# Kernel optimization log

Measured on AMD Instinct MI355X. Metric: run time of the kernel, lower is better.

## Reference

```python
import jax, jax.numpy as jnp
import numpy as np

D = 300      # embedding / model dim
H = 150      # LSTM hidden per direction (dim // 2)
V = 21257    # vocab size
B, S = 1024, 256


def _lstm_run(x, lengths, Wih, Whh, b):
    """Unidirectional masked LSTM. x: [B,S,Din]; outputs [B,S,H].
    State frozen and output zeroed at t >= lengths (packed-sequence semantics)."""
    Bb, Ss, _ = x.shape
    h0 = jnp.zeros((Bb, H), x.dtype)
    c0 = jnp.zeros((Bb, H), x.dtype)

    def step(carry, inp):
        h, c = carry
        xt, t = inp
        g = xt @ Wih.T + h @ Whh.T + b          # [B, 4H]
        i, f, gg, o = jnp.split(g, 4, axis=-1)   # torch gate order i,f,g,o
        i = jax.nn.sigmoid(i); f = jax.nn.sigmoid(f)
        gg = jnp.tanh(gg); o = jax.nn.sigmoid(o)
        c_new = f * c + i * gg
        h_new = o * jnp.tanh(c_new)
        valid = (t < lengths)[:, None]
        h2 = jnp.where(valid, h_new, h)
        c2 = jnp.where(valid, c_new, c)
        return (h2, c2), jnp.where(valid, h_new, jnp.zeros_like(h_new))

    _, ys = jax.lax.scan(step, (h0, c0), (jnp.swapaxes(x, 0, 1), jnp.arange(Ss)))
    return jnp.swapaxes(ys, 0, 1)


def _reverse_valid(x, lengths):
    """Reverse the valid prefix of each sequence; self-inverse on valid region."""
    Ss = x.shape[1]
    t = jnp.arange(Ss)[None, :]
    L = lengths[:, None]
    idx = jnp.where(t < L, L - 1 - t, t)
    return jnp.take_along_axis(x, idx[:, :, None], axis=1)


def _bilstm(x, lengths, pf, pb):
    hf = _lstm_run(x, lengths, *pf)
    hb = _reverse_valid(_lstm_run(_reverse_valid(x, lengths), lengths, *pb), lengths)
    return jnp.concatenate([hf, hb], axis=-1)  # [B,S,2H]


def setup_inputs() -> dict:
    key = jax.random.key(0)
    ks = jax.random.split(key, 20)
    x = jax.random.randint(ks[0], (B, S), 0, V)
    lengths = jax.random.randint(ks[1], (B,), 1, S + 1)
    mask = (jnp.arange(S)[None, :] < lengths[:, None]).astype(jnp.int64)

    def p(k, shape):
        return jax.random.normal(k, shape, dtype=jnp.float32) * 0.05

    emb = p(ks[2], (V, D))
    inp = {"x": x, "mask": mask, "emb": emb}
    # layer 0: input D; layer 1: input 2H (=D)
    names = [("l0f", D), ("l0b", D), ("l1f", 2 * H), ("l1b", 2 * H)]
    ki = 3
    for nm, din in names:
        inp[f"Wih_{nm}"] = p(ks[ki], (4 * H, din)); ki += 1
        inp[f"Whh_{nm}"] = p(ks[ki], (4 * H, H)); ki += 1
        inp[f"b_{nm}"] = p(ks[ki], (4 * H,)); ki += 1
    inp["W1"] = p(ks[15], (D, D)); inp["b1"] = p(ks[16], (D,))
    inp["W2"] = p(ks[17], (D, D)); inp["b2"] = p(ks[18], (D,))
    return inp


def reference(x, mask, emb,
              Wih_l0f, Whh_l0f, b_l0f, Wih_l0b, Whh_l0b, b_l0b,
              Wih_l1f, Whh_l1f, b_l1f, Wih_l1b, Whh_l1b, b_l1b,
              W1, b1, W2, b2):
    lengths = jnp.sum(mask != 0, axis=1)
    emb_z = emb.at[0].set(0.0)                 # padding_idx=0
    xe = emb_z[x]                              # [B,S,D]
    h1 = _bilstm(xe, lengths, (Wih_l0f, Whh_l0f, b_l0f), (Wih_l0b, Whh_l0b, b_l0b))
    h2 = _bilstm(h1, lengths, (Wih_l1f, Whh_l1f, b_l1f), (Wih_l1b, Whh_l1b, b_l1b))
    # gather output at last valid timestep (fwd last step || bwd first step)
    last = jnp.take_along_axis(h2, (lengths - 1)[:, None, None], axis=1)[:, 0, :]  # [B,300]
    # dropout is identity in eval mode
    out = jnp.tanh(last @ W1.T + b1)
    out = out @ W2.T + b2
    return out
```

## Files before the change

### kernel.cpp

```cpp
#include <hip/hip_runtime.h>

typedef unsigned short u16;
typedef __bf16 bf16x8 __attribute__((ext_vector_type(8)));
typedef float f32x4 __attribute__((ext_vector_type(4)));
typedef float f4 __attribute__((ext_vector_type(4)));
typedef unsigned short u16x8 __attribute__((ext_vector_type(8)));
typedef unsigned short u16x4 __attribute__((ext_vector_type(4)));

#define BB 1024
#define SS 256
#define DD 300
#define HH 150
#define GG 600
#define VV 21257
#define VPAD 21376
#define KSTR 320
#define GSTR 600
#define WK 160

static __device__ __forceinline__ float bf2f(u16 u){
  unsigned v = ((unsigned)u) << 16;
  return __builtin_bit_cast(float, v);
}
static __device__ __forceinline__ u16 f2bf(float f){
  unsigned u = __builtin_bit_cast(unsigned, f);
  u = u + 0x7FFFu + ((u >> 16) & 1u);
  return (u16)(u >> 16);
}
static __device__ __forceinline__ float fsig(float x){
  return __builtin_amdgcn_rcpf(1.0f + __expf(-x));
}
static __device__ __forceinline__ float ftanh_(float x){
  return 2.0f * __builtin_amdgcn_rcpf(1.0f + __expf(-2.0f*x)) - 1.0f;
}

__global__ void k_len(const int* __restrict__ mask, int* __restrict__ len){
  __shared__ int red[256];
  int b = blockIdx.x, t = threadIdx.x;
  red[t] = (mask[b*SS + t] != 0) ? 1 : 0;
  __syncthreads();
  for (int o = 128; o > 0; o >>= 1){
    if (t < o) red[t] += red[t+o];
    __syncthreads();
  }
  if (t == 0) len[b] = red[0];
}

__global__ void k_sort(const int* __restrict__ len, int* __restrict__ perm){
  __shared__ int L[1024];
  int b = threadIdx.x;
  int l = len[b];
  L[b] = l;
  __syncthreads();
  int r = 0;
  for (int j = 0; j < 1024; ++j){
    int lj = L[j];
    r += (lj < l) || (lj == l && j < b);
  }
  perm[r] = b;
}

struct PrepW {
  const float* src[8];
  u16* dst[8];
  int R[8], C[8], DR[8], DC[8];
};
__global__ void k_prepw(PrepW p){
  int z = blockIdx.y;
  int n = p.DR[z]*p.DC[z];
  for (int i = blockIdx.x*256 + threadIdx.x; i < n; i += 800*256){
    int r = i / p.DC[z], c = i - r*p.DC[z];
    float v = (r < p.R[z] && c < p.C[z]) ? p.src[z][r*p.C[z] + c] : 0.f;
    p.dst[z][i] = f2bf(v);
  }
}
struct PrepB { const float* src[4]; float* dst[4]; };
__global__ void k_prepb(PrepB p){
  int z = blockIdx.y;
  int i = blockIdx.x*256 + threadIdx.x;
  if (i < 640) p.dst[z][i] = (i < GG) ? p.src[z][i] : 0.f;
}

__global__ void k_prepemb(const float* __restrict__ emb, u16* __restrict__ dst){
  long i = (long)blockIdx.x*256 + threadIdx.x;
  if (i >= (long)VPAD*KSTR) return;
  int r = (int)(i / KSTR), c = (int)(i - (long)r*KSTR);
  float v = (r >= 1 && r < VV && c < DD) ? emb[(size_t)r*DD + c] : 0.f;
  dst[i] = f2bf(v);
}

__launch_bounds__(512, 2)
__global__ void k_gemm(const u16* __restrict__ A,
                       const u16* __restrict__ Wf, const u16* __restrict__ Wb,
                       const float* __restrict__ bsf, const float* __restrict__ bsb,
                       u16* __restrict__ of, u16* __restrict__ ob)
{
  const u16* W = blockIdx.z ? Wb : Wf;
  const float* bias = blockIdx.z ? bsb : bsf;
  u16* outp = blockIdx.z ? ob : of;

  __shared__ u16 Al[128*40];
  __shared__ u16 Bl[320*40];

  int tid = threadIdx.x;
  int l = tid & 63, w = tid >> 6;
  int lo = l & 15, hi = l >> 4;
  int wm = w >> 2, wn = w & 3;
  int m0 = blockIdx.x * 128;
  int n0 = blockIdx.y * 320;

  int ar = tid >> 2, ac = (tid & 3) * 8;
  const u16* Arow = A + (size_t)(m0 + ar)*KSTR + ac;
  bool bvld[3]; int brr[3], bcc[3];
  const u16* Brow[3];
  #pragma unroll
  for (int i = 0; i < 3; ++i){
    int ch = tid + i*512;
    bvld[i] = (ch < 1280);
    int r2 = bvld[i] ? (ch >> 2) : 0;
    brr[i] = r2; bcc[i] = (ch & 3) * 8;
    Brow[i] = W + (size_t)(n0 + r2)*KSTR + bcc[i];
  }

  u16x8 ra = *(const u16x8*)Arow;
  u16x8 rbv[3];
  #pragma unroll
  for (int i = 0; i < 3; ++i) if (bvld[i]) rbv[i] = *(const u16x8*)Brow[i];

  f32x4 zero = {0.f, 0.f, 0.f, 0.f};
  f32x4 acc[4][5];
  #pragma unroll
  for (int a = 0; a < 4; ++a)
    #pragma unroll
    for (int b = 0; b < 5; ++b) acc[a][b] = zero;

  for (int kk = 0; kk < 10; ++kk){
    __syncthreads();
    *(u16x8*)&Al[ar*40 + ac] = ra;
    #pragma unroll
    for (int i = 0; i < 3; ++i)
      if (bvld[i]) *(u16x8*)&Bl[brr[i]*40 + bcc[i]] = rbv[i];
    __syncthreads();
    if (kk < 9){
      int k1 = (kk+1)*32;
      ra = *(const u16x8*)(Arow + k1);
      #pragma unroll
      for (int i = 0; i < 3; ++i)
        if (bvld[i]) rbv[i] = *(const u16x8*)(Brow[i] + k1);
    }
    u16x8 av[4], bv[5];
    #pragma unroll
    for (int mt = 0; mt < 4; ++mt)
      av[mt] = *(const u16x8*)&Al[(wm*64 + mt*16 + lo)*40 + hi*8];
    #pragma unroll
    for (int nt = 0; nt < 5; ++nt)
      bv[nt] = *(const u16x8*)&Bl[(wn*80 + nt*16 + lo)*40 + hi*8];
    #pragma unroll
    for (int mt = 0; mt < 4; ++mt)
      #pragma unroll
      for (int nt = 0; nt < 5; ++nt)
        acc[mt][nt] = __builtin_amdgcn_mfma_f32_16x16x32_bf16(
            __builtin_bit_cast(bf16x8, av[mt]),
            __builtin_bit_cast(bf16x8, bv[nt]),
            acc[mt][nt], 0, 0, 0);
  }

  #pragma unroll
  for (int mt = 0; mt < 4; ++mt){
    #pragma unroll
    for (int nt = 0; nt < 5; ++nt){
      int col = n0 + wn*80 + nt*16 + lo;
      if (col < GG){
        float bsv = bias[col];
        int g = (col >= 450) ? 3 : (col >= 300) ? 2 : (col >= 150) ? 1 : 0;
        int cofs = (col - g*150)*4 + g;
        #pragma unroll
        for (int r = 0; r < 4; ++r){
          int row = m0 + wm*64 + mt*16 + hi*4 + r;
          outp[(size_t)row*GSTR + cofs] = f2bf(acc[mt][nt][r] + bsv);
        }
      }
    }
  }
}

#define PREF(GB, TT)                                                            \
  {                                                                             \
    _Pragma("unroll")                                                           \
    for (int r = 0; r < 4; ++r){                                                \
      int Li = Lr[r];                                                           \
      int tt = ((TT) < Li) ? (TT) : (Li-1);                                     \
      int s_ = dir ? (Li-1-tt) : tt;                                            \
      int tok = (int)tks[(hi*4+r)*256 + s_];                                    \
      int rowi = isL1 ? (rowb[r] + s_) : tok;                                   \
      GB[r] = *(const u16x4*)(xg + (size_t)rowi*GSTR + jjc*4);                  \
    }                                                                           \
  }

#define REC_STEP(T, PB, GB)                                                     \
  {                                                                             \
    f32x4 acc0 = {0,0,0,0}, acc1 = {0,0,0,0}, acc2 = {0,0,0,0}, acc3 = {0,0,0,0}; \
    __builtin_amdgcn_s_setprio(1);                                              \
    _Pragma("unroll")                                                           \
    for (int ks = 0; ks < 5; ++ks){                                             \
      u16x8 a_ = *(const u16x8*)&hsm[PB][lo*168 + ks*32 + hi*8];                \
      acc0 = __builtin_amdgcn_mfma_f32_16x16x32_bf16(                           \
          __builtin_bit_cast(bf16x8, a_), __builtin_bit_cast(bf16x8, bw[0][ks]), acc0, 0,0,0); \
      acc1 = __builtin_amdgcn_mfma_f32_16x16x32_bf16(                           \
          __builtin_bit_cast(bf16x8, a_), __builtin_bit_cast(bf16x8, bw[1][ks]), acc1, 0,0,0); \
      acc2 = __builtin_amdgcn_mfma_f32_16x16x32_bf16(                           \
          __builtin_bit_cast(bf16x8, a_), __builtin_bit_cast(bf16x8, bw[2][ks]), acc2, 0,0,0); \
      acc3 = __builtin_amdgcn_mfma_f32_16x16x32_bf16(                           \
          __builtin_bit_cast(bf16x8, a_), __builtin_bit_cast(bf16x8, bw[3][ks]), acc3, 0,0,0); \
    }                                                                           \
    __builtin_amdgcn_s_setprio(0);                                              \
    _Pragma("unroll")                                                           \
    for (int r = 0; r < 4; ++r){                                                \
      if (jv && (T) < Lr[r]){                                                   \
        float pi = acc0[r] + bf2f(GB[r][0]);                                    \
        float pf = acc1[r] + bf2f(GB[r][1]);                                    \
        float pg = acc2[r] + bf2f(GB[r][2]);                                    \
        float po = acc3[r] + bf2f(GB[r][3]);                                    \
        float ig = fsig(pi), fg = fsig(pf), g2 = ftanh_(pg), og = fsig(po);     \
        float cc = fg*cst[r] + ig*g2;  cst[r] = cc;                             \
        float hn = og * ftanh_(cc);                                             \
        u16 hb = f2bf(hn);                                                      \
        hsm[(PB)^1][(hi*4+r)*168 + jj] = hb;                                    \
        if (!isL1){                                                             \
          int s_ = dir ? (Lr[r]-1-(T)) : (T);                                   \
          h1[(size_t)(rowb[r]+s_)*KSTR + dir*150 + jj] = hb;                    \
        } else {                                                                \
          bool isl = dir ? ((T)==0) : ((T)==Lr[r]-1);                           \
          if (isl) lastf[(size_t)bo2[r]*304 + dir*150 + jj] = hn;               \
        }                                                                       \
      }                                                                         \
    }                                                                           \
    if ((T)+2 < maxL){                                                          \
      PREF(GB, (T)+2)                                                           \
    }                                                                           \
    __builtin_amdgcn_sched_barrier(0);                                          \
    asm volatile("s_waitcnt lgkmcnt(0)" ::: "memory");                          \
    __builtin_amdgcn_s_barrier();                                               \
    __builtin_amdgcn_sched_barrier(0);                                          \
  }

__launch_bounds__(640, 3)
__global__ void k_recM(const u16* __restrict__ gF, const u16* __restrict__ gBf,
                       const u16* __restrict__ tF, const u16* __restrict__ tB,
                       const u16* __restrict__ Wh0F, const u16* __restrict__ Wh0B,
                       const u16* __restrict__ Wh1F, const u16* __restrict__ Wh1B,
                       const int* __restrict__ len, const int* __restrict__ perm,
                       const int* __restrict__ x,
                       u16* __restrict__ h1, float* __restrict__ lastf,
                       int coA, int coB, int mode0)
{
  const int isL1 = (blockIdx.z == 0) ? mode0 : 0;
  const int dir  = blockIdx.y;
  const int tile = blockIdx.x;
  const int co   = isL1 ? coA : coB;
  const u16* xg  = isL1 ? (dir ? gBf : gF) : (dir ? tB : tF);
  const u16* Whh = isL1 ? (dir ? Wh1B : Wh1F) : (dir ? Wh0B : Wh0F);

  __shared__ u16 hsm[2][16*168];
  __shared__ u16 tks[16*256];
  __shared__ int Ls[16], rbL[16], boS[16];

  int tid = threadIdx.x;
  int l = tid & 63, w = tid >> 6;
  int lo = l & 15, hi = l >> 4;
  int jj = w*16 + lo;
  bool jv = (jj < HH);
  int jjc = jv ? jj : 0;

  u16x8 bw[4][5];
  #pragma unroll
  for (int g = 0; g < 4; ++g)
    #pragma unroll
    for (int ks = 0; ks < 5; ++ks)
      bw[g][ks] = *(const u16x8*)(Whh + (size_t)(g*150 + jj)*WK + ks*32 + hi*8);

  for (int i = tid; i < 2*16*168; i += 640) ((u16*)hsm)[i] = 0;
  if (tid < 16){
    int b = perm[co + tile*16 + tid];
    Ls[tid]  = len[b];
    rbL[tid] = (tile*16 + tid)*SS;
    boS[tid] = b;
  }
  __syncthreads();
  for (int idx = tid; idx < 16*256; idx += 640){
    int i = idx >> 8, s = idx & 255;
    tks[idx] = (u16)x[boS[i]*SS + s];
  }
  __syncthreads();

  int maxL = Ls[15];
  int Lr[4], rowb[4], bo2[4];
  #pragma unroll
  for (int r = 0; r < 4; ++r){
    int i = hi*4 + r;
    Lr[r] = Ls[i]; rowb[r] = rbL[i]; bo2[r] = boS[i];
  }

  float cst[4] = {0.f, 0.f, 0.f, 0.f};
  u16x4 gA[4], gB[4];
  PREF(gA, 0)
  PREF(gB, 1)
  asm volatile("s_waitcnt lgkmcnt(0)" ::: "memory");
  __builtin_amdgcn_s_barrier();

  for (int t = 0; t < maxL; t += 2){
    REC_STEP(t, 0, gA)
    if (t + 1 < maxL){
      REC_STEP(t+1, 1, gB)
    }
  }
}

__global__ void k_cls(const float* __restrict__ lastf,
                      const float* __restrict__ W1, const float* __restrict__ b1,
                      const float* __restrict__ W2, const float* __restrict__ b2,
                      float* __restrict__ out)
{
  __shared__ float inb[8][304];
  __shared__ float mid[8][304];
  int r0 = blockIdx.x * 8, tid = threadIdx.x;
  for (int i = tid; i < 8*76; i += 256){
    int r = i / 76, c4 = i - r*76;
    ((f4*)&inb[r][0])[c4] = ((const f4*)(lastf + (size_t)(r0+r)*304))[c4];
  }
  __syncthreads();
  for (int item = tid; item < 2400; item += 256){
    int r = item / 300, c = item - r*300;
    const f4* wr = (const f4*)(W1 + (size_t)c*300);
    const f4* xr = (const f4*)&inb[r][0];
    f4 a0 = {0,0,0,0}, a1 = {0,0,0,0}, a2 = {0,0,0,0};
    for (int k = 0; k < 75; k += 3){
      a0 += xr[k]   * wr[k];
      a1 += xr[k+1] * wr[k+1];
      a2 += xr[k+2] * wr[k+2];
    }
    f4 s4 = a0 + a1 + a2;
    float a = s4[0] + s4[1] + s4[2] + s4[3] + b1[c];
    mid[r][c] = ftanh_(a);
  }
  __syncthreads();
  for (int item = tid; item < 2400; item += 256){
    int r = item / 300, c = item - r*300;
    const f4* wr = (const f4*)(W2 + (size_t)c*300);
    const f4* xr = (const f4*)&mid[r][0];
    f4 a0 = {0,0,0,0}, a1 = {0,0,0,0}, a2 = {0,0,0,0};
    for (int k = 0; k < 75; k += 3){
      a0 += xr[k]   * wr[k];
      a1 += xr[k+1] * wr[k+1];
      a2 += xr[k+2] * wr[k+2];
    }
    f4 s4 = a0 + a1 + a2;
    out[(size_t)(r0+r)*300 + c] = s4[0] + s4[1] + s4[2] + s4[3] + b2[c];
  }
}

extern "C" void kernel_launch(void* const* d_in, const int* in_sizes, int n_in,
                              void* d_out, int out_size, void* d_ws, size_t ws_size,
                              hipStream_t stream)
{
  const int*   x    = (const int*)d_in[0];
  const int*   mask = (const int*)d_in[1];
  const float* emb  = (const float*)d_in[2];
  const float* Wih[4] = {(const float*)d_in[3], (const float*)d_in[6],
                         (const float*)d_in[9], (const float*)d_in[12]};
  const float* Whh[4] = {(const float*)d_in[4], (const float*)d_in[7],
                         (const float*)d_in[10], (const float*)d_in[13]};
  const float* bs[4]  = {(const float*)d_in[5], (const float*)d_in[8],
                         (const float*)d_in[11], (const float*)d_in[14]};
  const float* W1 = (const float*)d_in[15];
  const float* b1 = (const float*)d_in[16];
  const float* W2 = (const float*)d_in[17];
  const float* b2 = (const float*)d_in[18];
  float* out = (float*)d_out;

  char* p = (char*)d_ws;
  auto alloc = [&](size_t bytes){ char* r = p; p += (bytes + 255) & ~(size_t)255; return r; };

  u16 *WihP[4], *WhhP[4];
  for (int i = 0; i < 4; ++i){
    WihP[i] = (u16*)alloc(640*320*2);
    WhhP[i] = (u16*)alloc(640*160*2);
  }
  float* biasP[4];
  for (int i = 0; i < 4; ++i) biasP[i] = (float*)alloc(640*4);
  int* len  = (int*)alloc(1024*4);
  int* perm = (int*)alloc(1024*4);
  float* lastf = (float*)alloc((size_t)1024*304*4);
  u16* embP = (u16*)alloc((size_t)VPAD*KSTR*2);
  u16* tabF = (u16*)alloc((size_t)VPAD*GSTR*2);
  u16* tabB = (u16*)alloc((size_t)VPAD*GSTR*2);
  size_t fixed_end = (size_t)(p - (char*)d_ws);

  const size_t per_sample = (size_t)SS*KSTR*2 + 2*(size_t)SS*GSTR*2;
  int nc = 32;
  const int cands[6] = {1, 2, 4, 8, 16, 32};
  for (int ci = 0; ci < 6; ++ci){
    size_t need = fixed_end + (size_t)(BB / cands[ci]) * per_sample + (1u<<20);
    if (need <= ws_size){ nc = cands[ci]; break; }
  }
  const int Bc = BB / nc;
  const int Mc = Bc * SS;

  u16* h1    = (u16*)alloc((size_t)Mc*KSTR*2);
  u16* gateF = (u16*)alloc((size_t)Mc*GSTR*2);
  u16* gateB = (u16*)alloc((size_t)Mc*GSTR*2);

  hipMemsetAsync(h1, 0, (size_t)Mc*KSTR*2, stream);

  k_len <<<dim3(1024), dim3(256), 0, stream>>>(mask, len);
  k_sort<<<dim3(1),    dim3(1024),0, stream>>>(len, perm);

  PrepW pw;
  for (int i = 0; i < 4; ++i){
    pw.src[i] = Wih[i]; pw.dst[i] = WihP[i];
    pw.R[i] = GG; pw.C[i] = DD; pw.DR[i] = 640; pw.DC[i] = KSTR;
    pw.src[4+i] = Whh[i]; pw.dst[4+i] = WhhP[i];
    pw.R[4+i] = GG; pw.C[4+i] = HH; pw.DR[4+i] = 640; pw.DC[4+i] = WK;
  }
  k_prepw<<<dim3(800, 8), dim3(256), 0, stream>>>(pw);

  PrepB pb;
  for (int i = 0; i < 4; ++i){ pb.src[i] = bs[i]; pb.dst[i] = biasP[i]; }
  k_prepb<<<dim3(3, 4), dim3(256), 0, stream>>>(pb);

  k_prepemb<<<dim3((VPAD*KSTR + 255)/256), dim3(256), 0, stream>>>(emb, embP);

  k_gemm<<<dim3(VPAD/128, 2, 2), dim3(512), 0, stream>>>(embP, WihP[0], WihP[1],
                                                         biasP[0], biasP[1], tabF, tabB);

  k_recM<<<dim3(Bc/16, 2, 1), dim3(640), 0, stream>>>(gateF, gateB, tabF, tabB,
                                                      WhhP[0], WhhP[1], WhhP[2], WhhP[3],
                                                      len, perm, x, h1, lastf,
                                                      0, 0, 0);
  k_gemm<<<dim3(Mc/128, 2, 2), dim3(512), 0, stream>>>(h1, WihP[2], WihP[3],
                                                       biasP[2], biasP[3], gateF, gateB);
  for (int c = 0; c < nc; ++c){
    if (c + 1 < nc){
      k_recM<<<dim3(Bc/16, 2, 2), dim3(640), 0, stream>>>(gateF, gateB, tabF, tabB,
                                                          WhhP[0], WhhP[1], WhhP[2], WhhP[3],
                                                          len, perm, x, h1, lastf,
                                                          c*Bc, (c+1)*Bc, 1);
      k_gemm<<<dim3(Mc/128, 2, 2), dim3(512), 0, stream>>>(h1, WihP[2], WihP[3],
                                                           biasP[2], biasP[3], gateF, gateB);
    } else {
      k_recM<<<dim3(Bc/16, 2, 1), dim3(640), 0, stream>>>(gateF, gateB, tabF, tabB,
                                                          WhhP[0], WhhP[1], WhhP[2], WhhP[3],
                                                          len, perm, x, h1, lastf,
                                                          c*Bc, 0, 1);
    }
  }

  k_cls<<<dim3(128), dim3(256), 0, stream>>>(lastf, W1, b1, W2, b2, out);
}
```

Baseline: 3.646 ms.

## Fold log2e scaling into weights, deepen gate prefetch, drop setprio

Pre-scales the weights and biases by log2(e), or 2*log2(e) for the tanh gate rows, so the recurrent step can call exp2 directly without a multiply before each exp. It also deepens the gate-input prefetch from two to four timesteps with four register buffers, and removes the s_setprio calls around the MFMA block. The token table load is skipped for layer 1, and launch bounds drop from three to two blocks per CU to make room for the extra registers. The risks are lower occupancy and the bf16 rounding of the scaled weights, which changes numerics slightly. The scaling is applied in k_prepw by row index (300-449), so it assumes every prepared weight, including the layer-0 input weights, uses the same gate row layout.

New measurement: 3.483 ms. 4.5% less time.

```diff
diff --git a/kernel.cpp b/kernel.cpp
--- a/kernel.cpp
+++ b/kernel.cpp
@@ -17,6 +17,8 @@
 #define KSTR 320
 #define GSTR 600
 #define WK 160
+#define L2E 1.442695041f
+#define L2E2 2.885390082f
 
 static __device__ __forceinline__ float bf2f(u16 u){
   unsigned v = ((unsigned)u) << 16;
@@ -27,11 +29,11 @@
   u = u + 0x7FFFu + ((u >> 16) & 1u);
   return (u16)(u >> 16);
 }
-static __device__ __forceinline__ float fsig(float x){
-  return __builtin_amdgcn_rcpf(1.0f + __expf(-x));
-}
-static __device__ __forceinline__ float ftanh_(float x){
-  return 2.0f * __builtin_amdgcn_rcpf(1.0f + __expf(-2.0f*x)) - 1.0f;
+static __device__ __forceinline__ float fsig2(float p){
+  return __builtin_amdgcn_rcpf(1.0f + __builtin_amdgcn_exp2f(-p));
+}
+static __device__ __forceinline__ float ftanh2(float p){
+  return 2.0f * __builtin_amdgcn_rcpf(1.0f + __builtin_amdgcn_exp2f(-p)) - 1.0f;
 }
 
 __global__ void k_len(const int* __restrict__ mask, int* __restrict__ len){
@@ -71,14 +73,19 @@
   for (int i = blockIdx.x*256 + threadIdx.x; i < n; i += 800*256){
     int r = i / p.DC[z], c = i - r*p.DC[z];
     float v = (r < p.R[z] && c < p.C[z]) ? p.src[z][r*p.C[z] + c] : 0.f;
-    p.dst[z][i] = f2bf(v);
+    float sc = (r >= 300 && r < 450) ? L2E2 : L2E;
+    p.dst[z][i] = f2bf(v * sc);
   }
 }
 struct PrepB { const float* src[4]; float* dst[4]; };
 __global__ void k_prepb(PrepB p){
   int z = blockIdx.y;
   int i = blockIdx.x*256 + threadIdx.x;
-  if (i < 640) p.dst[z][i] = (i < GG) ? p.src[z][i] : 0.f;
+  if (i < 640){
+    float v = (i < GG) ? p.src[z][i] : 0.f;
+    float sc = (i >= 300 && i < 450) ? L2E2 : L2E;
+    p.dst[z][i] = v * sc;
+  }
 }
 
 __global__ void k_prepemb(const float* __restrict__ emb, u16* __restrict__ dst){
@@ -191,8 +198,9 @@
       int Li = Lr[r];                                                           \
       int tt = ((TT) < Li) ? (TT) : (Li-1);                                     \
       int s_ = dir ? (Li-1-tt) : tt;                                            \
-      int tok = (int)tks[(hi*4+r)*256 + s_];                                    \
-      int rowi = isL1 ? (rowb[r] + s_) : tok;                                   \
+      int rowi;                                                                 \
+      if (isL1) rowi = rowb[r] + s_;                                            \
+      else      rowi = (int)tks[(hi*4+r)*256 + s_];                             \
       GB[r] = *(const u16x4*)(xg + (size_t)rowi*GSTR + jjc*4);                  \
     }                                                                           \
   }
@@ -200,7 +208,6 @@
 #define REC_STEP(T, PB, GB)                                                     \
   {                                                                             \
     f32x4 acc0 = {0,0,0,0}, acc1 = {0,0,0,0}, acc2 = {0,0,0,0}, acc3 = {0,0,0,0}; \
-    __builtin_amdgcn_s_setprio(1);                                              \
     _Pragma("unroll")                                                           \
     for (int ks = 0; ks < 5; ++ks){                                             \
       u16x8 a_ = *(const u16x8*)&hsm[PB][lo*168 + ks*32 + hi*8];                \
@@ -213,7 +220,6 @@
       acc3 = __builtin_amdgcn_mfma_f32_16x16x32_bf16(                           \
           __builtin_bit_cast(bf16x8, a_), __builtin_bit_cast(bf16x8, bw[3][ks]), acc3, 0,0,0); \
     }                                                                           \
-    __builtin_amdgcn_s_setprio(0);                                              \
     _Pragma("unroll")                                                           \
     for (int r = 0; r < 4; ++r){                                                \
       if (jv && (T) < Lr[r]){                                                   \
@@ -221,9 +227,9 @@
         float pf = acc1[r] + bf2f(GB[r][1]);                                    \
         float pg = acc2[r] + bf2f(GB[r][2]);                                    \
         float po = acc3[r] + bf2f(GB[r][3]);                                    \
-        float ig = fsig(pi), fg = fsig(pf), g2 = ftanh_(pg), og = fsig(po);     \
+        float ig = fsig2(pi), fg = fsig2(pf), g2 = ftanh2(pg), og = fsig2(po);  \
         float cc = fg*cst[r] + ig*g2;  cst[r] = cc;                             \
-        float hn = og * ftanh_(cc);                                             \
+        float hn = og * ftanh2(L2E2 * cc);                                      \
         u16 hb = f2bf(hn);                                                      \
         hsm[(PB)^1][(hi*4+r)*168 + jj] = hb;                                    \
         if (!isL1){                                                             \
@@ -235,8 +241,8 @@
         }                                                                       \
       }                                                                         \
     }                                                                           \
-    if ((T)+2 < maxL){                                                          \
-      PREF(GB, (T)+2)                                                           \
+    if ((T)+4 < maxL){                                                          \
+      PREF(GB, (T)+4)                                                           \
     }                                                                           \
     __builtin_amdgcn_sched_barrier(0);                                          \
     asm volatile("s_waitcnt lgkmcnt(0)" ::: "memory");                          \
@@ -244,7 +250,7 @@
     __builtin_amdgcn_sched_barrier(0);                                          \
   }
 
-__launch_bounds__(640, 3)
+__launch_bounds__(640, 2)
 __global__ void k_recM(const u16* __restrict__ gF, const u16* __restrict__ gBf,
                        const u16* __restrict__ tF, const u16* __restrict__ tB,
                        const u16* __restrict__ Wh0F, const u16* __restrict__ Wh0B,
@@ -287,9 +293,11 @@
     boS[tid] = b;
   }
   __syncthreads();
-  for (int idx = tid; idx < 16*256; idx += 640){
-    int i = idx >> 8, s = idx & 255;
-    tks[idx] = (u16)x[boS[i]*SS + s];
+  if (!isL1){
+    for (int idx = tid; idx < 16*256; idx += 640){
+      int i = idx >> 8, s = idx & 255;
+      tks[idx] = (u16)x[boS[i]*SS + s];
+    }
   }
   __syncthreads();
 
@@ -302,17 +310,17 @@
   }
 
   float cst[4] = {0.f, 0.f, 0.f, 0.f};
-  u16x4 gA[4], gB[4];
-  PREF(gA, 0)
-  PREF(gB, 1)
-  asm volatile("s_waitcnt lgkmcnt(0)" ::: "memory");
-  __builtin_amdgcn_s_barrier();
-
-  for (int t = 0; t < maxL; t += 2){
-    REC_STEP(t, 0, gA)
-    if (t + 1 < maxL){
-      REC_STEP(t+1, 1, gB)
-    }
+  u16x4 g0[4], g1[4], g2b[4], g3[4];
+  PREF(g0, 0)
+  PREF(g1, 1)
+  PREF(g2b, 2)
+  PREF(g3, 3)
+
+  for (int t = 0; t < maxL; t += 4){
+    REC_STEP(t, 0, g0)
+    if (t + 1 < maxL) REC_STEP(t+1, 1, g1)
+    if (t + 2 < maxL) REC_STEP(t+2, 0, g2b)
+    if (t + 3 < maxL) REC_STEP(t+3, 1, g3)
   }
 }
 
@@ -341,7 +349,7 @@
     }
     f4 s4 = a0 + a1 + a2;
     float a = s4[0] + s4[1] + s4[2] + s4[3] + b1[c];
-    mid[r][c] = ftanh_(a);
+    mid[r][c] = 2.0f * __builtin_amdgcn_rcpf(1.0f + __builtin_amdgcn_exp2f(-L2E2*a)) - 1.0f;
   }
   __syncthreads();
   for (int item = tid; item < 2400; item += 256){
```
